# Kernel optimization log

Hardware: AMD Instinct MI355X
Metric: run time of the kernel (lower is better)

Reference implementation:

```python
import jax, jax.numpy as jnp
import numpy as np
from jax import lax

GAMMA = 1.5
ALPHA = 0.4
RADIUS = 2            # cv2 d=5 -> radius 2
SIGMA_COLOR = 0.05
SIGMA_SPACE = 50.0
BN_EPS = 1e-5


def setup_inputs() -> dict:
    key = jax.random.key(0)
    ks = jax.random.split(key, 6)
    B, C, H, W, F, L = 8, 1, 256, 256, 64, 15
    x = jax.random.normal(ks[0], (B, C, H, W), dtype=jnp.float32)
    w_init = jax.random.normal(ks[1], (F, C, 3, 3), dtype=jnp.float32) * 0.05
    w_body = jax.random.normal(ks[2], (L, F, F, 3, 3), dtype=jnp.float32) * 0.05
    bn_gamma = jnp.ones((L, F), dtype=jnp.float32) + 0.1 * jax.random.normal(ks[3], (L, F), dtype=jnp.float32)
    bn_beta = 0.1 * jax.random.normal(ks[4], (L, F), dtype=jnp.float32)
    w_final = jax.random.normal(ks[5], (C, F, 3, 3), dtype=jnp.float32) * 0.05
    return {"x": x, "w_init": w_init, "w_body": w_body,
            "bn_gamma": bn_gamma, "bn_beta": bn_beta, "w_final": w_final}


def _bilateral(img):
    # img: [B, H, W]; 5x5 bilateral filter, reflect-101 borders (cv2 default)
    r = RADIUS
    H, W = img.shape[1], img.shape[2]
    p = jnp.pad(img, ((0, 0), (r, r), (r, r)), mode='reflect')
    inv2sc = 1.0 / (2.0 * SIGMA_COLOR * SIGMA_COLOR)
    inv2ss = 1.0 / (2.0 * SIGMA_SPACE * SIGMA_SPACE)
    num = jnp.zeros_like(img)
    den = jnp.zeros_like(img)
    for dy in range(-r, r + 1):
        for dx in range(-r, r + 1):
            nb = p[:, dy + r:dy + r + H, dx + r:dx + r + W]
            sw = np.exp(-(dy * dy + dx * dx) * (1.0 / (2.0 * SIGMA_SPACE ** 2)))
            w = sw * jnp.exp(-(nb - img) ** 2 * inv2sc)
            num = num + w * nb
            den = den + w
    return num / den


def _preprocess(x):
    # x: [B, 1, H, W] in [-1, 1] nominal range
    xn = jnp.clip((x + 1.0) * 0.5, 1e-6, 1.0)
    img = xn[:, 0]                              # [B, H, W]
    blended = (1.0 - ALPHA) * img + ALPHA * jnp.power(img, GAMMA)
    return _bilateral(blended)[:, None]         # [B, 1, H, W]


def _conv(h, w):
    return lax.conv_general_dilated(h, w, (1, 1), 'SAME',
                                    dimension_numbers=('NCHW', 'OIHW', 'NCHW'))


def _dncnn(x_pre, w_init, w_body, bn_gamma, bn_beta, w_final):
    h = jax.nn.relu(_conv(x_pre, w_init))

    def body(h, params):
        w, g, b = params
        h = jax.nn.relu(_conv(h, w))
        mean = jnp.mean(h, axis=(0, 2, 3))
        var = jnp.var(h, axis=(0, 2, 3))
        h = (h - mean[None, :, None, None]) * jax.lax.rsqrt(var + BN_EPS)[None, :, None, None]
        h = h * g[None, :, None, None] + b[None, :, None, None]
        h = jax.nn.relu(h)
        return h, None

    h, _ = lax.scan(body, h, (w_body, bn_gamma, bn_beta))
    noise = _conv(h, w_final)
    return x_pre - noise


def reference(x, w_init, w_body, bn_gamma, bn_beta, w_final):
    x_pre = _preprocess(x)
    return _dncnn(x_pre, w_init, w_body, bn_gamma, bn_beta, w_final)
```

## Files before the change

kernel.cpp:

```cpp
#include <hip/hip_runtime.h>
#include <math.h>

#define B_   8
#define CH   64
#define H_   256
#define W_   256
#define NPIX (H_*W_)
#define NIMG (B_*NPIX)
#define NBLK 4096

typedef short bf16x8 __attribute__((ext_vector_type(8)));
typedef float f32x4  __attribute__((ext_vector_type(4)));

__device__ float g_stats[256];
__device__ float g_part[128 * NBLK];
__device__ __align__(16) short g_wpk[15 * 18 * 4 * 64 * 16];

__device__ __forceinline__ int refl(int i) {
    if (i < 0)    return -i;
    if (i >= 256) return 510 - i;
    return i;
}
__device__ __forceinline__ float prep1(float v) {
    float xn = fminf(fmaxf((v + 1.0f) * 0.5f, 1e-6f), 1.0f);
    return 0.6f * xn + 0.4f * xn * sqrtf(xn);
}
__device__ __forceinline__ unsigned short bf16_rne(float f) {
    union { float f; unsigned u; } v; v.f = f;
    unsigned r = v.u + 0x7FFFu + ((v.u >> 16) & 1u);
    return (unsigned short)(r >> 16);
}
__device__ __forceinline__ float bf16_f(unsigned short h) {
    union { float f; unsigned u; } v; v.u = ((unsigned)h) << 16;
    return v.f;
}
__device__ __forceinline__ unsigned cvt_pk_bf16(float a, float b) {
    unsigned r;
    asm volatile("v_cvt_pk_bf16_f32 %0, %1, %2" : "=v"(r) : "v"(a), "v"(b));
    return r;
}
__device__ __forceinline__ void bar_lds() {
    asm volatile("s_waitcnt lgkmcnt(0)" ::: "memory");
    __builtin_amdgcn_s_barrier();
}

__global__ void init_ab_kernel() {
    int c = threadIdx.x;
    g_stats[128 + c] = 1.0f;
    g_stats[192 + c] = 0.0f;
}

__global__ void prepack_kernel(const float* __restrict__ w_body) {
    int idx = blockIdx.x * 256 + threadIdx.x;
    if (idx >= 15*18*4*64) return;
    int lane = idx & 63;
    int m    = (idx >> 6) & 3;
    int r2   = idx >> 8;
    int l    = r2 / 18;
    int s    = r2 - l * 18;
    int t  = s >> 1;
    int oc = m * 16 + (lane & 15);
    int icb = (s & 1) * 32 + (lane >> 4) * 8;
    union { short s[8]; int4 v; } uh, ul;
    #pragma unroll
    for (int j = 0; j < 8; ++j) {
        float w = w_body[(((size_t)l * 64 + oc) * 64 + (icb + j)) * 9 + t];
        unsigned short h = bf16_rne(w);
        unsigned short lo = bf16_rne(w - bf16_f(h));
        uh.s[j] = (short)h;
        ul.s[j] = (short)lo;
    }
    int4* dst = (int4*)(g_wpk + (size_t)idx * 16);
    dst[0] = uh.v;
    dst[1] = ul.v;
}

__global__ __launch_bounds__(256) void conv_init_kernel(
    const float* __restrict__ x, const float* __restrict__ wi,
    float* __restrict__ h)
{
    __shared__ float s_bl[14][38];
    __shared__ float s_xp[10][34];
    __shared__ float s_w[64 * 12];
    int bx = blockIdx.x, by = blockIdx.y, b = blockIdx.z;
    int tid = threadIdx.x;
    const float* xb = x + b * NPIX;

    for (int i = tid; i < 14*38; i += 256) {
        int r = i / 38, c = i - r * 38;
        int gy = refl(by * 8 + r - 3), gx = refl(bx * 32 + c - 3);
        s_bl[r][c] = prep1(xb[gy * W_ + gx]);
    }
    for (int i = tid; i < 576; i += 256) {
        int oc = i / 9, t = i - oc * 9;
        s_w[oc * 12 + t] = wi[i];
    }
    __syncthreads();

    for (int i = tid; i < 10*34; i += 256) {
        int r = i / 34, c = i - r * 34;
        int gy = by * 8 + r - 1, gx = bx * 32 + c - 1;
        float v = 0.f;
        if (gy >= 0 && gy < H_ && gx >= 0 && gx < W_) {
            float ctr = s_bl[r + 2][c + 2];
            float num = 0.f, den = 0.f;
            #pragma unroll
            for (int dy = -2; dy <= 2; ++dy)
                #pragma unroll
                for (int dx = -2; dx <= 2; ++dx) {
                    float nb = s_bl[r + 2 + dy][c + 2 + dx];
                    float d  = nb - ctr;
                    float wgt = expf(-(float)(dy*dy + dx*dx) * 2e-4f - d * d * 200.0f);
                    num += wgt * nb;
                    den += wgt;
                }
            v = num / den;
        }
        s_xp[r][c] = v;
    }
    __syncthreads();

    int px = tid & 31, py = tid >> 5;
    float v[9];
    #pragma unroll
    for (int dr = 0; dr < 3; ++dr)
        #pragma unroll
        for (int dc = 0; dc < 3; ++dc)
            v[dr*3+dc] = s_xp[py + dr][px + dc];

    float acc[64];
    #pragma unroll
    for (int oc = 0; oc < 64; ++oc) {
        f32x4 w0 = *(const f32x4*)&s_w[oc * 12];
        f32x4 w1 = *(const f32x4*)&s_w[oc * 12 + 4];
        float w8 = s_w[oc * 12 + 8];
        float a = w0[0]*v[0] + w0[1]*v[1] + w0[2]*v[2] + w0[3]*v[3];
        a += w1[0]*v[4] + w1[1]*v[5] + w1[2]*v[6] + w1[3]*v[7];
        a = fmaf(w8, v[8], a);
        acc[oc] = fmaxf(a, 0.f);
    }

    int gy = by * 8 + py, gx = bx * 32 + px;
    float* outp = h + ((size_t)(b * NPIX + gy * W_ + gx)) * 64;
    #pragma unroll
    for (int c4 = 0; c4 < 16; ++c4) {
        float4 o = make_float4(acc[4*c4], acc[4*c4+1], acc[4*c4+2], acc[4*c4+3]);
        *reinterpret_cast<float4*>(outp + 4*c4) = o;
    }
}

__global__ __launch_bounds__(256, 4) void conv_body_mfma(
    const float* __restrict__ hin, int l, float* __restrict__ hout)
{
    __shared__ unsigned s_hi[180 * 20];
    __shared__ unsigned s_lo[180 * 20];

    int tid  = threadIdx.x;
    int lane = tid & 63;
    int wv   = tid >> 6;

    int bid = blockIdx.x;
    int swz = (bid & 7) * 512 + (bid >> 3);
    int bx = swz & 15;
    int by = (swz >> 4) & 31;
    int b  = swz >> 9;

    const float* ab = &g_stats[128];
    int q   = tid & 7;
    int c0  = q * 4;
    int pr0 = tid >> 3;

    f32x4 acc[4][2];
    #pragma unroll
    for (int m = 0; m < 4; ++m)
        #pragma unroll
        for (int n = 0; n < 2; ++n)
            acc[m][n] = (f32x4){0.f, 0.f, 0.f, 0.f};

    auto stage_chunk = [&](int chunk) {
        float4 a4 = *(const float4*)&ab[chunk * 32 + c0];
        float4 b4 = *(const float4*)&ab[64 + chunk * 32 + c0];
        #pragma unroll
        for (int k = 0; k < 6; ++k) {
            int p = k * 32 + pr0;
            if (p < 180) {
                int y = p / 18, xx = p - y * 18;
                int gy = by * 8 + y - 1, gx = bx * 16 + xx - 1;
                bool inb = (gy >= 0 && gy < H_ && gx >= 0 && gx < W_);
                const float4* src = (const float4*)(
                    hin + ((size_t)(b * NPIX + (inb ? gy * W_ + gx : 0))) * 64 + chunk * 32 + c0);
                float4 v = *src;
                float v0 = inb ? fmaxf(fmaf(v.x, a4.x, b4.x), 0.f) : 0.f;
                float v1 = inb ? fmaxf(fmaf(v.y, a4.y, b4.y), 0.f) : 0.f;
                float v2 = inb ? fmaxf(fmaf(v.z, a4.z, b4.z), 0.f) : 0.f;
                float v3 = inb ? fmaxf(fmaf(v.w, a4.w, b4.w), 0.f) : 0.f;
                unsigned hh0 = cvt_pk_bf16(v0, v1);
                unsigned hh1 = cvt_pk_bf16(v2, v3);
                float f0 = __uint_as_float(hh0 << 16);
                float f1 = __uint_as_float(hh0 & 0xffff0000u);
                float f2 = __uint_as_float(hh1 << 16);
                float f3 = __uint_as_float(hh1 & 0xffff0000u);
                unsigned ll0 = cvt_pk_bf16(v0 - f0, v1 - f1);
                unsigned ll1 = cvt_pk_bf16(v2 - f2, v3 - f3);
                *(uint2*)&s_hi[p * 20 + 2*q] = make_uint2(hh0, hh1);
                *(uint2*)&s_lo[p * 20 + 2*q] = make_uint2(ll0, ll1);
            }
        }
    };

    auto compute_chunk = [&](int chunk) {
        __builtin_amdgcn_s_setprio(1);
        #pragma unroll
        for (int t = 0; t < 9; ++t) {
            int s = 2 * t + chunk;
            const short* wb = g_wpk + ((size_t)(((l * 18 + s) * 4) * 64 + lane)) * 16;
            bf16x8 a_hi[4], a_lo[4];
            #pragma unroll
            for (int m = 0; m < 4; ++m) {
                const short* pw = wb + (size_t)m * 1024;
                a_hi[m] = *(const bf16x8*)(pw);
                a_lo[m] = *(const bf16x8*)(pw + 8);
            }
            int dr = t / 3, dc = t - dr * 3;
            #pragma unroll
            for (int n = 0; n < 2; ++n) {
                int y = 2 * wv + n + dr;
                int p = y * 18 + dc + (lane & 15);
                int woff = p * 20 + (lane >> 4) * 4;
                bf16x8 b_hi = *(const bf16x8*)&s_hi[woff];
                bf16x8 b_lo = *(const bf16x8*)&s_lo[woff];
                #pragma unroll
                for (int m = 0; m < 4; ++m) {
                    acc[m][n] = __builtin_amdgcn_mfma_f32_16x16x32_bf16(a_hi[m], b_hi, acc[m][n], 0, 0, 0);
                    acc[m][n] = __builtin_amdgcn_mfma_f32_16x16x32_bf16(a_hi[m], b_lo, acc[m][n], 0, 0, 0);
                    acc[m][n] = __builtin_amdgcn_mfma_f32_16x16x32_bf16(a_lo[m], b_hi, acc[m][n], 0, 0, 0);
                }
            }
        }
        __builtin_amdgcn_s_setprio(0);
    };

    int ck0 = (bid >> 8) & 1;
    stage_chunk(ck0);
    bar_lds();
    compute_chunk(ck0);
    bar_lds();
    stage_chunk(ck0 ^ 1);
    bar_lds();
    compute_chunk(ck0 ^ 1);

    bar_lds();
    float* s_red = (float*)s_hi;

    int q4  = lane >> 4;
    int gxs = bx * 16 + (lane & 15);
    float ps1[4][4], ps2[4][4];
    #pragma unroll
    for (int m = 0; m < 4; ++m)
        #pragma unroll
        for (int r = 0; r < 4; ++r) { ps1[m][r] = 0.f; ps2[m][r] = 0.f; }

    #pragma unroll
    for (int n = 0; n < 2; ++n) {
        int gy = by * 8 + 2 * wv + n;
        float* op = hout + ((size_t)(b * NPIX + gy * W_ + gxs)) * 64 + q4 * 4;
        #pragma unroll
        for (int m = 0; m < 4; ++m) {
            float a0 = fmaxf(acc[m][n][0], 0.f);
            float a1 = fmaxf(acc[m][n][1], 0.f);
            float a2 = fmaxf(acc[m][n][2], 0.f);
            float a3 = fmaxf(acc[m][n][3], 0.f);
            *reinterpret_cast<float4*>(op + m * 16) = make_float4(a0, a1, a2, a3);
            ps1[m][0] += a0; ps1[m][1] += a1; ps1[m][2] += a2; ps1[m][3] += a3;
            ps2[m][0] += a0*a0; ps2[m][1] += a1*a1; ps2[m][2] += a2*a2; ps2[m][3] += a3*a3;
        }
    }
    #pragma unroll
    for (int m = 0; m < 4; ++m) {
        #pragma unroll
        for (int r = 0; r < 4; ++r) {
            float a = ps1[m][r], s = ps2[m][r];
            #pragma unroll
            for (int off = 1; off < 16; off <<= 1) {
                a += __shfl_xor(a, off);
                s += __shfl_xor(s, off);
            }
            if ((lane & 15) == 0) {
                int oc = m * 16 + q4 * 4 + r;
                s_red[(wv * 64 + oc) * 2]     = a;
                s_red[(wv * 64 + oc) * 2 + 1] = s;
            }
        }
    }
    __syncthreads();
    if (tid < 128) {
        float v = s_red[tid] + s_red[128 + tid] + s_red[256 + tid] + s_red[384 + tid];
        g_part[(size_t)tid * NBLK + bid] = v;
    }
}

__global__ __launch_bounds__(256) void bn_finalize_kernel(
    const float* __restrict__ gamma, const float* __restrict__ beta)
{
    __shared__ float s[8];
    int c = blockIdx.x;
    int t = threadIdx.x;
    const float* p1 = g_part + (size_t)(2 * c) * NBLK;
    const float* p2 = g_part + (size_t)(2 * c + 1) * NBLK;
    float s1 = 0.f, s2 = 0.f;
    for (int i = t; i < NBLK; i += 256) { s1 += p1[i]; s2 += p2[i]; }
    #pragma unroll
    for (int off = 32; off >= 1; off >>= 1) {
        s1 += __shfl_xor(s1, off);
        s2 += __shfl_xor(s2, off);
    }
    int lane = t & 63, w = t >> 6;
    if (lane == 0) { s[w * 2] = s1; s[w * 2 + 1] = s2; }
    __syncthreads();
    if (t == 0) {
        float sum = s[0] + s[2] + s[4] + s[6];
        float sq  = s[1] + s[3] + s[5] + s[7];
        const float invN = 1.0f / (float)NIMG;
        float mean = sum * invN;
        float var  = sq * invN - mean * mean;
        float a = gamma[c] / sqrtf(var + 1e-5f);
        g_stats[128 + c] = a;
        g_stats[192 + c] = beta[c] - mean * a;
    }
}

__global__ __launch_bounds__(256) void conv_final_kernel(
    const float* __restrict__ hin, const float* __restrict__ wf,
    const float* __restrict__ x, float* __restrict__ out)
{
    __shared__ float s_in[324 * 36];
    __shared__ float s_bl[20][21];
    __shared__ float s_w[64 * 12];
    int bx = blockIdx.x, by = blockIdx.y, b = blockIdx.z;
    int tid = threadIdx.x;
    const float* xb = x + b * NPIX;
    const float* ab = &g_stats[128];

    for (int i = tid; i < 20*20; i += 256) {
        int r = i / 20, c = i - r * 20;
        int gy = refl(by * 16 + r - 2), gx = refl(bx * 16 + c - 2);
        s_bl[r][c] = prep1(xb[gy * W_ + gx]);
    }
    for (int i = tid; i < 576; i += 256) {
        int ic = i / 9, t = i - ic * 9;
        s_w[ic * 12 + t] = wf[i];
    }
    __syncthreads();

    int px = tid & 15, py = tid >> 4;
    float ctr = s_bl[py + 2][px + 2];
    float num = 0.f, den = 0.f;
    #pragma unroll
    for (int dy = -2; dy <= 2; ++dy)
        #pragma unroll
        for (int dx = -2; dx <= 2; ++dx) {
            float nb = s_bl[py + 2 + dy][px + 2 + dx];
            float d  = nb - ctr;
            float wgt = expf(-(float)(dy*dy + dx*dx) * 2e-4f - d * d * 200.0f);
            num += wgt * nb;
            den += wgt;
        }
    float xpre = num / den;

    int q   = tid & 7;
    int c0  = q * 4;
    int pr0 = tid >> 3;
    float acc = 0.f;

    for (int chunk = 0; chunk < 2; ++chunk) {
        __syncthreads();
        float4 a4 = *(const float4*)&ab[chunk * 32 + c0];
        float4 b4 = *(const float4*)&ab[64 + chunk * 32 + c0];
        #pragma unroll
        for (int k = 0; k < 11; ++k) {
            int p = k * 32 + pr0;
            if (p < 324) {
                int y = p / 18, xx = p - y * 18;
                int gy = by * 16 + y - 1, gx = bx * 16 + xx - 1;
                bool inb = (gy >= 0 && gy < H_ && gx >= 0 && gx < W_);
                const float4* src = (const float4*)(
                    hin + ((size_t)(b * NPIX + (inb ? gy * W_ + gx : 0))) * 64 + chunk * 32 + c0);
                float4 v = *src;
                float4 o;
                o.x = inb ? fmaxf(fmaf(v.x, a4.x, b4.x), 0.f) : 0.f;
                o.y = inb ? fmaxf(fmaf(v.y, a4.y, b4.y), 0.f) : 0.f;
                o.z = inb ? fmaxf(fmaf(v.z, a4.z, b4.z), 0.f) : 0.f;
                o.w = inb ? fmaxf(fmaf(v.w, a4.w, b4.w), 0.f) : 0.f;
                *(float4*)&s_in[p * 36 + 4*q] = o;
            }
        }
        __syncthreads();

        #pragma unroll
        for (int u = 0; u < 8; ++u) {
            f32x4 wreg[4][3];
            #pragma unroll
            for (int e = 0; e < 4; ++e)
                #pragma unroll
                for (int g = 0; g < 3; ++g)
                    wreg[e][g] = *(const f32x4*)&s_w[(chunk * 32 + u * 4 + e) * 12 + g * 4];
            #pragma unroll
            for (int t = 0; t < 9; ++t) {
                int dr = t / 3, dc = t - dr * 3;
                const float4 hv = *(const float4*)&s_in[((py + dr) * 18 + px + dc) * 36 + 4 * u];
                acc = fmaf(hv.x, wreg[0][t >> 2][t & 3], acc);
                acc = fmaf(hv.y, wreg[1][t >> 2][t & 3], acc);
                acc = fmaf(hv.z, wreg[2][t >> 2][t & 3], acc);
                acc = fmaf(hv.w, wreg[3][t >> 2][t & 3], acc);
            }
        }
    }

    int gy = by * 16 + py, gx = bx * 16 + px;
    out[b * NPIX + gy * W_ + gx] = xpre - acc;
}

extern "C" void kernel_launch(void* const* d_in, const int* in_sizes, int n_in,
                              void* d_out, int out_size, void* d_ws, size_t ws_size,
                              hipStream_t stream)
{
    const float* x        = (const float*)d_in[0];
    const float* w_init   = (const float*)d_in[1];
    const float* w_body   = (const float*)d_in[2];
    const float* bn_gamma = (const float*)d_in[3];
    const float* bn_beta  = (const float*)d_in[4];
    const float* w_final  = (const float*)d_in[5];
    float* out = (float*)d_out;

    char* wsb = (char*)d_ws;
    float* hA = (float*)wsb;
    float* hB = (float*)(wsb + 134217728ULL);

    init_ab_kernel <<<1, 64, 0, stream>>>();
    prepack_kernel <<<270, 256, 0, stream>>>(w_body);
    conv_init_kernel<<<dim3(8, 32, 8), 256, 0, stream>>>(x, w_init, hA);

    float* cur = hA;
    float* nxt = hB;
    for (int l = 0; l < 15; ++l) {
        conv_body_mfma<<<NBLK, 256, 0, stream>>>(cur, l, nxt);
        bn_finalize_kernel<<<64, 256, 0, stream>>>(bn_gamma + l * 64, bn_beta + l * 64);
        float* tp = cur; cur = nxt; nxt = tp;
    }
    conv_final_kernel<<<dim3(16, 16, 8), 256, 0, stream>>>(cur, w_final, x, out);
}
```

Baseline: 2.196 ms.

## Stage both channel chunks into LDS at once before a single MFMA pass

The body convolution kernel now loads and converts both 32-channel halves of the input halo tile into a wider LDS tile (row stride 34 dwords) in one phase. It then runs all 18 tap/chunk MFMA steps after a single barrier. The old stage-compute-stage-compute sequence with its chunk-order stagger is gone. This removes two barriers and exposes more global loads in flight at once. In exchange, LDS per block roughly doubles, which may cut resident blocks per CU below the launch-bounds target, and the stagger that spread blocks across channel halves is dropped.

```diff
diff --git a/kernel.cpp b/kernel.cpp
--- a/kernel.cpp
+++ b/kernel.cpp
@@ -8,6 +8,7 @@
 #define NPIX (H_*W_)
 #define NIMG (B_*NPIX)
 #define NBLK 4096
+#define PS   34
 
 typedef short bf16x8 __attribute__((ext_vector_type(8)));
 typedef float f32x4  __attribute__((ext_vector_type(4)));
@@ -152,8 +153,8 @@
 __global__ __launch_bounds__(256, 4) void conv_body_mfma(
     const float* __restrict__ hin, int l, float* __restrict__ hout)
 {
-    __shared__ unsigned s_hi[180 * 20];
-    __shared__ unsigned s_lo[180 * 20];
+    __shared__ unsigned s_hi[180 * PS];
+    __shared__ unsigned s_lo[180 * PS];
 
     int tid  = threadIdx.x;
     int lane = tid & 63;
@@ -177,9 +178,10 @@
         for (int n = 0; n < 2; ++n)
             acc[m][n] = (f32x4){0.f, 0.f, 0.f, 0.f};
 
-    auto stage_chunk = [&](int chunk) {
-        float4 a4 = *(const float4*)&ab[chunk * 32 + c0];
-        float4 b4 = *(const float4*)&ab[64 + chunk * 32 + c0];
+    #pragma unroll
+    for (int c = 0; c < 2; ++c) {
+        float4 a4 = *(const float4*)&ab[c * 32 + c0];
+        float4 b4 = *(const float4*)&ab[64 + c * 32 + c0];
         #pragma unroll
         for (int k = 0; k < 6; ++k) {
             int p = k * 32 + pr0;
@@ -188,7 +190,7 @@
                 int gy = by * 8 + y - 1, gx = bx * 16 + xx - 1;
                 bool inb = (gy >= 0 && gy < H_ && gx >= 0 && gx < W_);
                 const float4* src = (const float4*)(
-                    hin + ((size_t)(b * NPIX + (inb ? gy * W_ + gx : 0))) * 64 + chunk * 32 + c0);
+                    hin + ((size_t)(b * NPIX + (inb ? gy * W_ + gx : 0))) * 64 + c * 32 + c0);
                 float4 v = *src;
                 float v0 = inb ? fmaxf(fmaf(v.x, a4.x, b4.x), 0.f) : 0.f;
                 float v1 = inb ? fmaxf(fmaf(v.y, a4.y, b4.y), 0.f) : 0.f;
@@ -202,17 +204,20 @@
                 float f3 = __uint_as_float(hh1 & 0xffff0000u);
                 unsigned ll0 = cvt_pk_bf16(v0 - f0, v1 - f1);
                 unsigned ll1 = cvt_pk_bf16(v2 - f2, v3 - f3);
-                *(uint2*)&s_hi[p * 20 + 2*q] = make_uint2(hh0, hh1);
-                *(uint2*)&s_lo[p * 20 + 2*q] = make_uint2(ll0, ll1);
-            }
-        }
-    };
-
-    auto compute_chunk = [&](int chunk) {
-        __builtin_amdgcn_s_setprio(1);
+                *(uint2*)&s_hi[p * PS + c * 16 + 2*q] = make_uint2(hh0, hh1);
+                *(uint2*)&s_lo[p * PS + c * 16 + 2*q] = make_uint2(ll0, ll1);
+            }
+        }
+    }
+
+    bar_lds();
+
+    __builtin_amdgcn_s_setprio(1);
+    #pragma unroll
+    for (int c = 0; c < 2; ++c) {
         #pragma unroll
         for (int t = 0; t < 9; ++t) {
-            int s = 2 * t + chunk;
+            int s = 2 * t + c;
             const short* wb = g_wpk + ((size_t)(((l * 18 + s) * 4) * 64 + lane)) * 16;
             bf16x8 a_hi[4], a_lo[4];
             #pragma unroll
@@ -226,7 +231,7 @@
             for (int n = 0; n < 2; ++n) {
                 int y = 2 * wv + n + dr;
                 int p = y * 18 + dc + (lane & 15);
-                int woff = p * 20 + (lane >> 4) * 4;
+                int woff = p * PS + c * 16 + (lane >> 4) * 4;
                 bf16x8 b_hi = *(const bf16x8*)&s_hi[woff];
                 bf16x8 b_lo = *(const bf16x8*)&s_lo[woff];
                 #pragma unroll
@@ -237,17 +242,8 @@
                 }
             }
         }
-        __builtin_amdgcn_s_setprio(0);
-    };
-
-    int ck0 = (bid >> 8) & 1;
-    stage_chunk(ck0);
-    bar_lds();
-    compute_chunk(ck0);
-    bar_lds();
-    stage_chunk(ck0 ^ 1);
-    bar_lds();
-    compute_chunk(ck0 ^ 1);
+    }
+    __builtin_amdgcn_s_setprio(0);
 
     bar_lds();
     float* s_red = (float*)s_hi;
```

After: 2.418 ms. +10.1%, slower.
